# Optimization experiments

Measured on AMD Instinct MI355X. Metric: run time of the kernel, lower is better.

Reference implementation:

```python
import jax, jax.numpy as jnp
import numpy as np

B, H, W = 128, 64, 64
CH = 64            # feature channels (hardcoded self.channels=64)
GH = GW = 8        # glimpse size
HID = 128          # controller_out
NUM_GLIMPSES = 8
BN_EPS = 1e-5


def setup_inputs() -> dict:
    key = jax.random.key(0)
    ks = jax.random.split(key, 16)
    d = {}
    d['image_pairs'] = jax.random.normal(ks[0], (B, 2, H, W), dtype=jnp.float32)
    # ResidualBlock(1 -> 64)
    d['conv1_w'] = jax.random.normal(ks[1], (CH, 1, 3, 3), jnp.float32) * 0.1
    d['conv1_b'] = jnp.zeros((CH,), jnp.float32)
    d['bn1_g'] = jnp.ones((CH,), jnp.float32)
    d['bn1_b'] = jnp.zeros((CH,), jnp.float32)
    d['conv2_w'] = jax.random.normal(ks[2], (CH, CH, 3, 3), jnp.float32) * 0.02
    d['conv2_b'] = jnp.zeros((CH,), jnp.float32)
    d['bn2_g'] = jnp.ones((CH,), jnp.float32)
    d['bn2_b'] = jnp.zeros((CH,), jnp.float32)
    # LSTMCell(input=GH*GW*CH=4096, hidden=128); torch gate order i,f,g,o
    in_sz = GH * GW * CH
    d['w_ih'] = jax.random.normal(ks[3], (4 * HID, in_sz), jnp.float32) * 0.01
    d['w_hh'] = jax.random.normal(ks[4], (4 * HID, HID), jnp.float32) * 0.05
    d['b_ih'] = jnp.zeros((4 * HID,), jnp.float32)
    d['b_hh'] = jnp.zeros((4 * HID,), jnp.float32)
    # glimpser Linear(128 -> 3)
    d['glimpser_w'] = jax.random.normal(ks[5], (3, HID), jnp.float32) * 0.05
    d['glimpser_b'] = jnp.zeros((3,), jnp.float32)
    return d


def _conv3x3(x, w, b):
    # x: (B,C,H,W), w: (O,I,3,3) -> SAME padding, stride 1 (NCHW/OIHW)
    y = jax.lax.conv_general_dilated(x, w, (1, 1), 'SAME',
                                     dimension_numbers=('NCHW', 'OIHW', 'NCHW'))
    return y + b[None, :, None, None]


def _bn(x, g, b):
    # BatchNorm2d in training mode: batch statistics over (N,H,W)
    m = jnp.mean(x, axis=(0, 2, 3), keepdims=True)
    v = jnp.var(x, axis=(0, 2, 3), keepdims=True)
    return (x - m) * jax.lax.rsqrt(v + BN_EPS) * g[None, :, None, None] + b[None, :, None, None]


def _resblock(x, c1w, c1b, g1, b1, c2w, c2b, g2, b2):
    out = jax.nn.relu(_bn(_conv3x3(x, c1w, c1b), g1, b1))
    out = _bn(_conv3x3(out, c2w, c2b), g2, b2)
    # residual add broadcasts (B,1,H,W) -> (B,64,H,W), matching torch
    return jax.nn.relu(out + x)


def _filterbank(delta_caps, center_caps, image_size, glimpse_size):
    # returns (B, glimpse_size, image_size) Cauchy filterbank
    S = float(image_size)
    G = float(glimpse_size)
    centers = (S - 1.0) * (center_caps + 1.0) / 2.0          # (B,)
    deltas = S / G * (1.0 - jnp.abs(delta_caps))             # (B,)
    gammas = jnp.exp(1.0 - 2.0 * jnp.abs(delta_caps))        # (B,)
    gp = jnp.arange(glimpse_size, dtype=jnp.float32) - (G - 1.0) / 2.0
    gp = centers[:, None] + deltas[:, None] * gp[None, :]    # (B, g)
    ip = jnp.arange(image_size, dtype=jnp.float32)           # (S,)
    fx = (ip[None, None, :] - gp[:, :, None]) / gammas[:, None, None]
    fx = 1.0 / (jnp.pi * gammas[:, None, None] * (1.0 + fx * fx))  # (B, g, S)
    fx = fx / (jnp.sum(fx, axis=2, keepdims=True) + 1e-4)
    return fx


def reference(image_pairs, conv1_w, conv1_b, bn1_g, bn1_b,
              conv2_w, conv2_b, bn2_g, bn2_b,
              w_ih, w_hh, b_ih, b_hh, glimpser_w, glimpser_b):
    image_pairs = image_pairs.astype(jnp.float32)
    support = _resblock(image_pairs[:, 0:1], conv1_w, conv1_b, bn1_g, bn1_b,
                        conv2_w, conv2_b, bn2_g, bn2_b)  # (B,64,H,W)
    test = _resblock(image_pairs[:, 1:2], conv1_w, conv1_b, bn1_g, bn1_b,
                     conv2_w, conv2_b, bn2_g, bn2_b)
    bsz = image_pairs.shape[0]
    Hx = jnp.zeros((bsz, HID), jnp.float32)
    Cx = jnp.zeros((bsz, HID), jnp.float32)
    for turn in range(2 * NUM_GLIMPSES):
        imgs = support if (turn % 2) else test
        gp = jnp.tanh(Hx @ glimpser_w.T + glimpser_b)        # (B,3)
        Fh = _filterbank(gp[:, 2], gp[:, 0], imgs.shape[2], GH)  # (B,gh,H)
        Fw = _filterbank(gp[:, 2], gp[:, 1], imgs.shape[3], GW)  # (B,gw,W)
        # glimpse = Fh . image . Fw^T per channel (fused contraction)
        t = jnp.einsum('bgi,bcij->bcgj', Fh, imgs)           # (B,C,gh,W)
        gl = jnp.einsum('bcgj,bwj->bcgw', t, Fw)             # (B,C,gh,gw)
        flat = gl.reshape(bsz, -1)                           # (B, C*gh*gw)
        gates = flat @ w_ih.T + b_ih + Hx @ w_hh.T + b_hh    # (B, 4*HID)
        i, f, g, o = jnp.split(gates, 4, axis=1)
        Cx = jax.nn.sigmoid(f) * Cx + jax.nn.sigmoid(i) * jnp.tanh(g)
        Hx = jax.nn.sigmoid(o) * jnp.tanh(Cx)
    return Hx
```

## Files before the change

### kernel.cpp

```cpp
#include <hip/hip_runtime.h>
#include <math.h>

typedef unsigned short u16;
typedef unsigned int u32;
typedef short bf16x8 __attribute__((ext_vector_type(8)));
typedef float f32x4 __attribute__((ext_vector_type(4)));

#define PI_F 3.14159265358979323846f

__device__ __forceinline__ float bf2f(u16 u){ union{u32 i; float f;} v; v.i=((u32)u)<<16; return v.f; }
__device__ __forceinline__ u16 f2bf(float f){ union{u32 i; float f;} v; v.f=f; u32 r=v.i+0x7fffu+((v.i>>16)&1u); return (u16)(r>>16); }
__device__ __forceinline__ float sigf(float x){ return 1.0f/(1.0f+expf(-x)); }

__global__ __launch_bounds__(256) void wpack_kernel(const float* __restrict__ w2, u16* __restrict__ wpack)
{
  int e = blockIdx.x*256 + threadIdx.x;
  if (e >= 36864) return;
  int k  = e & 31;
  int oc = (e>>5) & 63;
  int tc = e>>11;
  int tap = tc>>1, c = tc&1;
  int ic = c*32 + k;
  wpack[e] = f2bf(w2[(size_t)(oc*64 + ic)*9 + tap]);
}

__global__ __launch_bounds__(256) void conv1_nhwc_kernel(
    const float* __restrict__ imgp, int ch,
    const float* __restrict__ w1, u16* __restrict__ out)
{
  int b = blockIdx.y, tile = blockIdx.x;
  int ty0 = (tile>>2)<<4, tx0 = (tile&3)<<4;
  int tid = threadIdx.x;
  __shared__ float patch[18*18];
  __shared__ float wsm[576];
  const float* ib = imgp + (((size_t)b*2 + ch)<<12);
  for (int e=tid; e<324; e+=256){
    int py = e/18, px = e - py*18;
    int gy = ty0+py-1, gx = tx0+px-1;
    float v = 0.f;
    if (gy>=0 && gy<64 && gx>=0 && gx<64) v = ib[(gy<<6)+gx];
    patch[e] = v;
  }
  for (int e=tid; e<576; e+=256) wsm[e] = w1[e];
  __syncthreads();
  int ty = tid>>4, tx = tid&15;
  float p[9];
  #pragma unroll
  for (int ky=0;ky<3;ky++)
    #pragma unroll
    for (int kx=0;kx<3;kx++) p[ky*3+kx] = patch[(ty+ky)*18 + tx+kx];
  u16* ob = out + ((((size_t)b<<12) + ((size_t)(ty0+ty)<<6) + (size_t)(tx0+tx))<<6);
  #pragma unroll
  for (int ocq=0; ocq<8; ocq++){
    u32 w4[4];
    #pragma unroll
    for (int pair=0; pair<4; pair++){
      float a0=0.f, a1=0.f;
      int oc0 = ocq*8 + pair*2;
      #pragma unroll
      for (int k=0;k<9;k++){ a0 += wsm[oc0*9+k]*p[k]; a1 += wsm[(oc0+1)*9+k]*p[k]; }
      w4[pair] = (u32)f2bf(a0) | ((u32)f2bf(a1)<<16);
    }
    ((uint4*)ob)[ocq] = make_uint4(w4[0],w4[1],w4[2],w4[3]);
  }
}

__device__ __forceinline__ void stats_body(const u16* __restrict__ buf, float* __restrict__ st, int blk, int tid)
{
  int c8 = (tid&7)*8;
  int pg = tid>>3;
  size_t p0 = (size_t)blk*1024 + pg;
  float s[8], s2[8];
  #pragma unroll
  for (int k=0;k<8;k++){ s[k]=0.f; s2[k]=0.f; }
  for (int it=0; it<32; it++){
    size_t p = p0 + (size_t)it*32;
    uint4 v = *(const uint4*)(buf + (p<<6) + c8);
    u32 rw[4] = {v.x,v.y,v.z,v.w};
    #pragma unroll
    for (int d=0; d<4; d++){
      float f0 = bf2f((u16)(rw[d]&0xffff));
      float f1 = bf2f((u16)(rw[d]>>16));
      s[d*2]   += f0; s2[d*2]   += f0*f0;
      s[d*2+1] += f1; s2[d*2+1] += f1*f1;
    }
  }
  #pragma unroll
  for (int off=32; off>=8; off>>=1){
    #pragma unroll
    for (int k=0;k<8;k++){ s[k] += __shfl_down(s[k], off, 64); s2[k] += __shfl_down(s2[k], off, 64); }
  }
  __shared__ float sm[128];
  if (tid<128) sm[tid]=0.f;
  __syncthreads();
  if ((tid&63) < 8){
    int cb = tid&7;
    #pragma unroll
    for (int k=0;k<8;k++){
      atomicAdd(&sm[cb*8+k], s[k]);
      atomicAdd(&sm[64+cb*8+k], s2[k]);
    }
  }
  __syncthreads();
  if (tid<128) atomicAdd(&st[tid], sm[tid]);
}

__global__ __launch_bounds__(256) void stats_nhwc_kernel(const u16* __restrict__ buf, float* __restrict__ st)
{
  stats_body(buf, st, blockIdx.x, threadIdx.x);
}

__global__ __launch_bounds__(256) void stats_pair_kernel(
    const u16* __restrict__ A, const u16* __restrict__ B,
    float* __restrict__ stA, float* __restrict__ stB)
{
  const u16* buf = (blockIdx.x < 512)? A : B;
  float* st = (blockIdx.x < 512)? stA : stB;
  stats_body(buf, st, blockIdx.x & 511, threadIdx.x);
}

__global__ __launch_bounds__(256) void conv2_mfma_kernel(
    const u16* __restrict__ in, const u16* __restrict__ wpack, u16* __restrict__ out,
    const float* __restrict__ st, const float* __restrict__ gam, const float* __restrict__ bet)
{
  int b = blockIdx.y, tile = blockIdx.x;
  int y0 = (tile>>2)*8, x0 = (tile&3)*16;
  int tid = threadIdx.x;
  int w = tid>>6, lane = tid&63;
  int m = lane&15, q = lane>>4;

  __shared__ __align__(16) u16 patch[11520];
  __shared__ float scs[64], shs[64];

  if (tid < 64){
    const float invN = 1.0f/524288.0f;
    float mean = st[tid]*invN;
    float var  = st[64+tid]*invN - mean*mean;
    float sc = gam[tid]*rsqrtf(var+1e-5f);
    scs[tid] = sc;
    shs[tid] = bet[tid] - mean*sc;
  }
  __syncthreads();

  for (int e=tid; e<1440; e+=256){
    int py = e/144; int rem = e - py*144;
    int px = rem>>3, cq = rem&7;
    int y = y0-1+py, x = x0-1+px;
    uint4 v = make_uint4(0,0,0,0);
    if (y>=0 && y<64 && x>=0 && x<64){
      uint4 raw = *(const uint4*)(in + ((((size_t)b<<12) + ((size_t)y<<6) + (size_t)x)<<6) + cq*8);
      u32 rw[4] = {raw.x, raw.y, raw.z, raw.w};
      u32 ow[4];
      #pragma unroll
      for (int d=0; d<4; d++){
        u32 o = 0;
        #pragma unroll
        for (int h=0; h<2; h++){
          int c = cq*8 + d*2 + h;
          float f = bf2f((u16)((rw[d]>>(16*h))&0xffff))*scs[c] + shs[c];
          f = fmaxf(f, 0.f);
          o |= ((u32)f2bf(f)) << (16*h);
        }
        ow[d] = o;
      }
      v = make_uint4(ow[0],ow[1],ow[2],ow[3]);
    }
    *(uint4*)(patch + ((((py<<3)+cq)*18 + px)<<3)) = v;
  }
  __syncthreads();

  f32x4 acc[2][4];
  #pragma unroll
  for (int mt=0;mt<2;mt++)
    #pragma unroll
    for (int nt=0;nt<4;nt++) acc[mt][nt] = (f32x4){0.f,0.f,0.f,0.f};

  #pragma unroll
  for (int tap=0; tap<9; tap++){
    const int dy = tap/3, dx = tap%3;
    #pragma unroll
    for (int c=0; c<2; c++){
      const int kk = tap*2 + c;
      bf16x8 bw[4];
      #pragma unroll
      for (int nt=0; nt<4; nt++)
        bw[nt] = *(const bf16x8*)(wpack + (size_t)(kk*64 + nt*16 + m)*32 + q*8);
      #pragma unroll
      for (int mt=0; mt<2; mt++){
        int py = 2*w + mt + dy;
        bf16x8 av = *(const bf16x8*)(patch + ((((py<<3) + (c<<2) + q)*18 + (m+dx))<<3));
        #pragma unroll
        for (int nt=0; nt<4; nt++)
          acc[mt][nt] = __builtin_amdgcn_mfma_f32_16x16x32_bf16(av, bw[nt], acc[mt][nt], 0,0,0);
      }
    }
  }
  __syncthreads();
  u16* etile = patch;
  #pragma unroll
  for (int mt=0; mt<2; mt++){
    int lp = (2*w+mt)*16 + q*4;
    #pragma unroll
    for (int nt=0; nt<4; nt++)
      #pragma unroll
      for (int r=0; r<4; r++)
        etile[(lp+r)*64 + nt*16 + m] = f2bf(acc[mt][nt][r]);
  }
  __syncthreads();
  int lp = tid>>1, half = tid&1;
  int y = y0 + (lp>>4), x = x0 + (lp&15);
  uint4* gdst = (uint4*)(out + ((((size_t)b<<12) + ((size_t)y<<6) + (size_t)x)<<6) + half*32);
  const uint4* lsrc = (const uint4*)(etile + lp*64 + half*32);
  gdst[0] = lsrc[0];
  gdst[1] = lsrc[1];
  gdst[2] = lsrc[2];
  gdst[3] = lsrc[3];
}

__device__ __forceinline__ void compute_params_lane(
    int b, int lane, float h0, float h1,
    const float* __restrict__ gw, const float* __restrict__ gb,
    float* __restrict__ FhT, float* __restrict__ Fw)
{
  float gpv[3];
  #pragma unroll
  for (int k=0;k<3;k++){
    float p = h0*gw[k*128+lane] + h1*gw[k*128+64+lane];
    #pragma unroll
    for (int off=32; off>0; off>>=1) p += __shfl_down(p, off, 64);
    float tot = __shfl(p, 0, 64);
    gpv[k] = tanhf(tot + gb[k]);
  }
  float ad = fabsf(gpv[2]);
  float delta = 8.0f*(1.0f-ad);
  float gamma = expf(1.0f-2.0f*ad);
  float inv_pg = 1.0f/(PI_F*gamma);
  float fi = (float)lane;
  float ctr = 31.5f*(gpv[0]+1.0f);
  float fh[8];
  #pragma unroll
  for (int g=0; g<8; g++){
    float mu = ctr + delta*((float)g - 3.5f);
    float u = (fi - mu)/gamma;
    float f = inv_pg/(1.0f+u*u);
    float s = f;
    #pragma unroll
    for (int off=32; off>0; off>>=1) s += __shfl_down(s, off, 64);
    s = __shfl(s, 0, 64);
    fh[g] = f/(s + 1e-4f);
  }
  float4* o = (float4*)(FhT + (((size_t)b<<6) + lane)*8);
  o[0] = make_float4(fh[0],fh[1],fh[2],fh[3]);
  o[1] = make_float4(fh[4],fh[5],fh[6],fh[7]);
  ctr = 31.5f*(gpv[1]+1.0f);
  #pragma unroll
  for (int wv=0; wv<8; wv++){
    float mu = ctr + delta*((float)wv - 3.5f);
    float u = (fi - mu)/gamma;
    float f = inv_pg/(1.0f+u*u);
    float s = f;
    #pragma unroll
    for (int off=32; off>0; off>>=1) s += __shfl_down(s, off, 64);
    s = __shfl(s, 0, 64);
    Fw[(((size_t)b<<3)+wv)*64 + lane] = f/(s + 1e-4f);
  }
}

__device__ __forceinline__ void compute_params_lds(
    int lane, int jc, const float* __restrict__ hnew,
    const float* __restrict__ gw, const float* __restrict__ gb,
    float* __restrict__ fh_lds, float* __restrict__ fw_lds)
{
  float h0 = hnew[lane], h1 = hnew[64+lane];
  float gpv[3];
  #pragma unroll
  for (int k=0;k<3;k++){
    float p = h0*gw[k*128+lane] + h1*gw[k*128+64+lane];
    #pragma unroll
    for (int off=32; off>0; off>>=1) p += __shfl_down(p, off, 64);
    float tot = __shfl(p, 0, 64);
    gpv[k] = tanhf(tot + gb[k]);
  }
  float ad = fabsf(gpv[2]);
  float delta = 8.0f*(1.0f-ad);
  float gamma = expf(1.0f-2.0f*ad);
  float inv_pg = 1.0f/(PI_F*gamma);
  float fi = (float)lane;
  float ctr = 31.5f*(gpv[0]+1.0f);
  #pragma unroll
  for (int g=0; g<8; g++){
    float mu = ctr + delta*((float)g - 3.5f);
    float u = (fi - mu)/gamma;
    float f = inv_pg/(1.0f+u*u);
    float s = f;
    #pragma unroll
    for (int off=32; off>0; off>>=1) s += __shfl_down(s, off, 64);
    s = __shfl(s, 0, 64);
    fh_lds[lane*8+g] = f/(s + 1e-4f);
  }
  ctr = 31.5f*(gpv[1]+1.0f);
  #pragma unroll
  for (int wv=0; wv<8; wv++){
    float mu = ctr + delta*((float)wv - 3.5f);
    float u = (fi - mu)/gamma;
    float f = inv_pg/(1.0f+u*u);
    float s = f;
    #pragma unroll
    for (int off=32; off>0; off>>=1) s += __shfl_down(s, off, 64);
    s = __shfl(s, 0, 64);
    int jl = lane - jc*16;
    if (jl >= 0 && jl < 16) fw_lds[jl*8+wv] = f/(s + 1e-4f);
  }
}

__global__ __launch_bounds__(256) void glimpse_lstm_kernel(
    const u16* __restrict__ img, const float* __restrict__ part,
    const float* __restrict__ whhT,
    const float* __restrict__ bih, const float* __restrict__ bhh,
    const float* __restrict__ gw, const float* __restrict__ gb,
    const float* __restrict__ Hx_in, const float* __restrict__ Cx_in,
    float* __restrict__ Hx_out, float* __restrict__ Cx_out,
    float* __restrict__ part_gl,
    const float* __restrict__ st2, const float* __restrict__ gam2,
    const float* __restrict__ bet2, const float* __restrict__ imgp,
    int ch, int t)
{
  int jc = blockIdx.x, b = blockIdx.y;
  int tid = threadIdx.x;
  __shared__ float hs[128];
  __shared__ float hnew[128];
  __shared__ float gsm[512];
  __shared__ float scs[64], shs[64];
  __shared__ __align__(16) float fh_lds[512];
  __shared__ __align__(16) float fw_lds[128];
  __shared__ __align__(16) float t_lds[8*16*64];

  if (tid < 64){
    const float invN = 1.0f/524288.0f;
    float mean = st2[tid]*invN;
    float var  = st2[64+tid]*invN - mean*mean;
    float sc = gam2[tid]*rsqrtf(var+1e-5f);
    scs[tid] = sc;
    shs[tid] = bet2[tid] - mean*sc;
  }

  if (t > 0){
    if (tid < 128) hs[tid] = Hx_in[b*128+tid];
    __syncthreads();
    #pragma unroll
    for (int gq=0; gq<2; gq++){
      int n = gq*256 + tid;
      float acc = bih[n] + bhh[n];
      const float* pp = part + (size_t)b*16384 + n;
      #pragma unroll 8
      for (int ks=0; ks<32; ks++) acc += pp[ks*512];
      const float* wp = whhT + n;
      #pragma unroll 8
      for (int k=0;k<128;k++) acc += hs[k]*wp[(size_t)k*512];
      gsm[n] = acc;
    }
    __syncthreads();
    if (tid < 128){
      float cx = Cx_in[b*128+tid];
      float cn = sigf(gsm[128+tid])*cx + sigf(gsm[tid])*tanhf(gsm[256+tid]);
      float hn = sigf(gsm[384+tid])*tanhf(cn);
      hnew[tid] = hn;
      if (jc == 0){ Cx_out[b*128+tid] = cn; Hx_out[b*128+tid] = hn; }
    }
  } else {
    if (tid < 128) hnew[tid] = 0.f;
  }
  __syncthreads();

  if (tid < 64) compute_params_lds(tid, jc, hnew, gw, gb, fh_lds, fw_lds);
  __syncthreads();

  int ih = tid>>7, j = (tid>>3)&15, cg = tid&7;
  float scq[8], shq[8];
  #pragma unroll
  for (int k=0;k<8;k++){ scq[k] = scs[cg*8+k]; shq[k] = shs[cg*8+k]; }
  f32x4 accA[8], accB[8];
  #pragma unroll
  for (int g=0;g<8;g++){ accA[g]=(f32x4){0.f,0.f,0.f,0.f}; accB[g]=(f32x4){0.f,0.f,0.f,0.f}; }
  const u16* ib = img + ((((size_t)b<<12) + ((size_t)(ih*32)<<6) + (size_t)(jc*16+j))<<6) + cg*8;
  const float* rp = imgp + (((size_t)(b*2+ch))<<12) + ((size_t)(ih*32)<<6) + (jc*16+j);
  #pragma unroll 8
  for (int ii=0; ii<32; ii++){
    uint4 vv = *(const uint4*)(ib + ((size_t)ii<<12));
    float res = rp[ii<<6];
    float x0=fmaxf(bf2f((u16)(vv.x&0xffff))*scq[0]+shq[0]+res, 0.f);
    float x1=fmaxf(bf2f((u16)(vv.x>>16))   *scq[1]+shq[1]+res, 0.f);
    float x2=fmaxf(bf2f((u16)(vv.y&0xffff))*scq[2]+shq[2]+res, 0.f);
    float x3=fmaxf(bf2f((u16)(vv.y>>16))   *scq[3]+shq[3]+res, 0.f);
    float x4=fmaxf(bf2f((u16)(vv.z&0xffff))*scq[4]+shq[4]+res, 0.f);
    float x5=fmaxf(bf2f((u16)(vv.z>>16))   *scq[5]+shq[5]+res, 0.f);
    float x6=fmaxf(bf2f((u16)(vv.w&0xffff))*scq[6]+shq[6]+res, 0.f);
    float x7=fmaxf(bf2f((u16)(vv.w>>16))   *scq[7]+shq[7]+res, 0.f);
    int i = ih*32+ii;
    f32x4 fa = *(const f32x4*)&fh_lds[i*8];
    f32x4 fb = *(const f32x4*)&fh_lds[i*8+4];
    #pragma unroll
    for (int g=0;g<4;g++){
      accA[g][0]+=fa[g]*x0; accA[g][1]+=fa[g]*x1; accA[g][2]+=fa[g]*x2; accA[g][3]+=fa[g]*x3;
      accB[g][0]+=fa[g]*x4; accB[g][1]+=fa[g]*x5; accB[g][2]+=fa[g]*x6; accB[g][3]+=fa[g]*x7;
      accA[g+4][0]+=fb[g]*x0; accA[g+4][1]+=fb[g]*x1; accA[g+4][2]+=fb[g]*x2; accA[g+4][3]+=fb[g]*x3;
      accB[g+4][0]+=fb[g]*x4; accB[g+4][1]+=fb[g]*x5; accB[g+4][2]+=fb[g]*x6; accB[g+4][3]+=fb[g]*x7;
    }
  }
  if (ih==0){
    #pragma unroll
    for (int g=0;g<8;g++){
      *(f32x4*)&t_lds[(g*16+j)*64 + cg*8]     = accA[g];
      *(f32x4*)&t_lds[(g*16+j)*64 + cg*8 + 4] = accB[g];
    }
  }
  __syncthreads();
  if (ih==1){
    #pragma unroll
    for (int g=0;g<8;g++){
      f32x4* p0 = (f32x4*)&t_lds[(g*16+j)*64 + cg*8];
      p0[0] = p0[0] + accA[g];
      p0[1] = p0[1] + accB[g];
    }
  }
  __syncthreads();

  int c = tid&63, s = tid>>6;
  float acc2[2][8];
  #pragma unroll
  for (int gi=0;gi<2;gi++)
    #pragma unroll
    for (int wv=0;wv<8;wv++) acc2[gi][wv]=0.f;
  #pragma unroll
  for (int jl=0; jl<16; jl++){
    float tv0 = t_lds[((((s*2  )<<4)+jl)<<6) + c];
    float tv1 = t_lds[((((s*2+1)<<4)+jl)<<6) + c];
    f32x4 w0 = *(const f32x4*)&fw_lds[jl*8];
    f32x4 w1 = *(const f32x4*)&fw_lds[jl*8+4];
    acc2[0][0]+=tv0*w0[0]; acc2[0][1]+=tv0*w0[1]; acc2[0][2]+=tv0*w0[2]; acc2[0][3]+=tv0*w0[3];
    acc2[0][4]+=tv0*w1[0]; acc2[0][5]+=tv0*w1[1]; acc2[0][6]+=tv0*w1[2]; acc2[0][7]+=tv0*w1[3];
    acc2[1][0]+=tv1*w0[0]; acc2[1][1]+=tv1*w0[1]; acc2[1][2]+=tv1*w0[2]; acc2[1][3]+=tv1*w0[3];
    acc2[1][4]+=tv1*w1[0]; acc2[1][5]+=tv1*w1[1]; acc2[1][6]+=tv1*w1[2]; acc2[1][7]+=tv1*w1[3];
  }
  float* dst = part_gl + (((size_t)(b*4+jc))<<12) + c*64 + (s*2)*8;
  *(f32x4*)(dst+0)  = (f32x4){acc2[0][0],acc2[0][1],acc2[0][2],acc2[0][3]};
  *(f32x4*)(dst+4)  = (f32x4){acc2[0][4],acc2[0][5],acc2[0][6],acc2[0][7]};
  *(f32x4*)(dst+8)  = (f32x4){acc2[1][0],acc2[1][1],acc2[1][2],acc2[1][3]};
  *(f32x4*)(dst+12) = (f32x4){acc2[1][4],acc2[1][5],acc2[1][6],acc2[1][7]};
}

__global__ __launch_bounds__(256) void gemm_ih_kernel(
    const float* __restrict__ part_gl, const float* __restrict__ Bw, float* __restrict__ part)
{
  int n0 = blockIdx.x*64;
  int kb = blockIdx.y;
  int k0 = kb*128;
  __shared__ __align__(16) float Asm[16*132];
  __shared__ __align__(16) float Bsm[16*68];
  int tid = threadIdx.x;
  int tm = tid & 15, tn = tid >> 4;
  float acc[8][4];
  #pragma unroll
  for (int i=0;i<8;i++)
    #pragma unroll
    for (int jj=0;jj<4;jj++) acc[i][jj]=0.f;
  for (int kt=0; kt<128; kt+=16){
    for (int e=tid; e<512; e+=256){
      int mrow = e>>2, kq = e&3;
      const float* pg = part_gl + ((size_t)mrow<<14) + (k0+kt+kq*4);
      float4 a0 = *(const float4*)pg;
      float4 a1 = *(const float4*)(pg+4096);
      float4 a2 = *(const float4*)(pg+8192);
      float4 a3 = *(const float4*)(pg+12288);
      float4 a = make_float4(a0.x+a1.x+a2.x+a3.x, a0.y+a1.y+a2.y+a3.y,
                             a0.z+a1.z+a2.z+a3.z, a0.w+a1.w+a2.w+a3.w);
      Asm[(kq*4+0)*132+mrow] = a.x;
      Asm[(kq*4+1)*132+mrow] = a.y;
      Asm[(kq*4+2)*132+mrow] = a.z;
      Asm[(kq*4+3)*132+mrow] = a.w;
    }
    {
      int e = tid;
      int n = e>>2, kq = e&3;
      float4 bv = *(const float4*)(Bw + (size_t)(n0+n)*4096 + k0+kt+kq*4);
      Bsm[(kq*4+0)*68+n] = bv.x;
      Bsm[(kq*4+1)*68+n] = bv.y;
      Bsm[(kq*4+2)*68+n] = bv.z;
      Bsm[(kq*4+3)*68+n] = bv.w;
    }
    __syncthreads();
    #pragma unroll
    for (int kk=0;kk<16;kk++){
      float4 bv = *(const float4*)&Bsm[kk*68 + tn*4];
      float4 a0 = *(const float4*)&Asm[kk*132 + tm*8];
      float4 a1 = *(const float4*)&Asm[kk*132 + tm*8 + 4];
      float av[8] = {a0.x,a0.y,a0.z,a0.w,a1.x,a1.y,a1.z,a1.w};
      #pragma unroll
      for (int mm=0;mm<8;mm++){
        acc[mm][0] += av[mm]*bv.x;
        acc[mm][1] += av[mm]*bv.y;
        acc[mm][2] += av[mm]*bv.z;
        acc[mm][3] += av[mm]*bv.w;
      }
    }
    __syncthreads();
  }
  #pragma unroll
  for (int mm=0;mm<8;mm++){
    int mrow = tm*8+mm;
    *(float4*)&part[(size_t)mrow*16384 + kb*512 + n0 + tn*4] =
        make_float4(acc[mm][0],acc[mm][1],acc[mm][2],acc[mm][3]);
  }
}

__global__ __launch_bounds__(256) void lstm_update_kernel(
    float* __restrict__ Hx, float* __restrict__ Cx,
    const float* __restrict__ part, const float* __restrict__ whhT,
    const float* __restrict__ b_ih, const float* __restrict__ b_hh,
    const float* __restrict__ gw, const float* __restrict__ gb,
    float* __restrict__ FhT, float* __restrict__ Fw)
{
  int b = blockIdx.x;
  int tid = threadIdx.x;
  int hid = tid & 127, half = tid >> 7;
  __shared__ float hs[128];
  __shared__ float hs2[128];
  __shared__ float gp[1024];
  if (tid < 128) hs[tid] = Hx[b*128+tid];
  __syncthreads();
  #pragma unroll
  for (int qd=0; qd<4; qd++){
    int n = qd*128 + hid;
    float acc = half ? 0.f : (b_ih[n] + b_hh[n]);
    const float* pp = part + (size_t)b*16384 + (size_t)(half*16)*512 + n;
    #pragma unroll
    for (int ks=0; ks<16; ks++) acc += pp[ks*512];
    const float* wp = whhT + n + (size_t)(half*64)*512;
    const float* hp = hs + half*64;
    #pragma unroll 8
    for (int k=0;k<64;k++) acc += hp[k]*wp[(size_t)k*512];
    gp[(half*4+qd)*128 + hid] = acc;
  }
  __syncthreads();
  if (tid < 128){
    float g0 = gp[  0+tid] + gp[512+  0+tid];
    float g1 = gp[128+tid] + gp[512+128+tid];
    float g2 = gp[256+tid] + gp[512+256+tid];
    float g3 = gp[384+tid] + gp[512+384+tid];
    float cx = Cx[b*128+tid];
    float cn = sigf(g1)*cx + sigf(g0)*tanhf(g2);
    float hn = sigf(g3)*tanhf(cn);
    Cx[b*128+tid] = cn;
    Hx[b*128+tid] = hn;
    hs2[tid] = hn;
  }
  __syncthreads();
  if (tid < 64)
    compute_params_lane(b, tid, hs2[tid], hs2[64+tid], gw, gb, FhT, Fw);
}

__global__ __launch_bounds__(256) void transpose_whh_kernel(
    const float* __restrict__ whh, float* __restrict__ whhT)
{
  int idx = blockIdx.x*256 + threadIdx.x;
  int k = idx>>9, n = idx&511;
  whhT[idx] = whh[n*128 + k];
}

extern "C" void kernel_launch(void* const* d_in, const int* in_sizes, int n_in,
                              void* d_out, int out_size, void* d_ws, size_t ws_size,
                              hipStream_t stream)
{
  const float* imgp = (const float*)d_in[0];
  const float* w1  = (const float*)d_in[1];
  const float* g1  = (const float*)d_in[3];
  const float* be1 = (const float*)d_in[4];
  const float* w2  = (const float*)d_in[5];
  const float* g2  = (const float*)d_in[7];
  const float* be2 = (const float*)d_in[8];
  const float* wih = (const float*)d_in[9];
  const float* whh = (const float*)d_in[10];
  const float* bih = (const float*)d_in[11];
  const float* bhh = (const float*)d_in[12];
  const float* gw  = (const float*)d_in[13];
  const float* gb  = (const float*)d_in[14];

  char* ws = (char*)d_ws;
  u16* imgT    = (u16*)(ws + 0);
  u16* imgS    = (u16*)(ws + 67108864);
  u16* tmp     = (u16*)(ws + 134217728);
  float* Hbuf1   = (float*)(ws + 134217728);
  float* cbuf1   = (float*)(ws + 134283264);
  float* part_gl = (float*)(ws + 134742016);
  float* part    = (float*)(ws + 143130624);
  float* whhT    = (float*)(ws + 151519232);
  u16*   wpack   = (u16*)  (ws + 201326592);
  float* Hbuf0   = (float*)(ws + 201400320);
  float* cbuf0   = (float*)(ws + 201465856);
  float* stats   = (float*)(ws + 201531392);
  if (ws_size < 201533440ull) return;

  hipMemsetAsync(Hbuf0, 0, 65536+65536+2048, stream);
  wpack_kernel<<<144,256,0,stream>>>(w2, wpack);

  for (int s=0; s<2; s++){
    int ch = (s==0)?1:0;
    u16* dst = (s==0)? imgT : imgS;
    conv1_nhwc_kernel<<<dim3(16,128),256,0,stream>>>(imgp, ch, w1, tmp);
    stats_nhwc_kernel<<<512,256,0,stream>>>(tmp, stats + 128*(2*s));
    conv2_mfma_kernel<<<dim3(32,128),256,0,stream>>>(tmp, wpack, dst,
        stats + 128*(2*s), g1, be1);
  }
  stats_pair_kernel<<<1024,256,0,stream>>>(imgT, imgS, stats + 128, stats + 384);

  transpose_whh_kernel<<<256,256,0,stream>>>(whh, whhT);

  for (int t=0; t<16; t++){
    int sup = t&1;
    const u16* im = sup? imgS : imgT;
    const float* st2 = sup? (stats+384) : (stats+128);
    int ch = sup? 0 : 1;
    const float* Hin = sup? Hbuf0 : Hbuf1;
    const float* Cin = sup? cbuf0 : cbuf1;
    float* Hout = sup? Hbuf1 : Hbuf0;
    float* Cout = sup? cbuf1 : cbuf0;
    glimpse_lstm_kernel<<<dim3(4,128),256,0,stream>>>(
        im, part, whhT, bih, bhh, gw, gb, Hin, Cin, Hout, Cout, part_gl,
        st2, g2, be2, imgp, ch, t);
    gemm_ih_kernel<<<dim3(8,32),256,0,stream>>>(part_gl, wih, part);
  }
  lstm_update_kernel<<<128,256,0,stream>>>(Hbuf1, cbuf1, part, whhT, bih, bhh, gw, gb,
                                           part_gl, part_gl + 65536 );

  hipMemcpyAsync(d_out, Hbuf1, (size_t)16384*4, hipMemcpyDeviceToDevice, stream);
}
```

Before: 1.511 ms.

## Shrink per-block work in conv2, glimpse and input GEMM kernels to add parallelism

The conv2 MFMA kernel now covers 4-row tiles instead of 8, with each wave computing one row, and launches twice as many blocks. The glimpse/LSTM kernel moves to 512 threads, so each thread handles 16 rows instead of 32 and the extra partial sums are reduced through LDS. The input-projection GEMM halves its N tile to 32 and doubles its grid. The aim is higher occupancy and more blocks on a latency-bound pipeline, at the cost of more halo loads, extra LDS reduction passes with barriers, and less reuse per block.

```diff
diff --git a/kernel.cpp b/kernel.cpp
--- a/kernel.cpp
+++ b/kernel.cpp
@@ -119,17 +119,17 @@
   stats_body(buf, st, blockIdx.x & 511, threadIdx.x);
 }
 
-__global__ __launch_bounds__(256) void conv2_mfma_kernel(
+__global__ __launch_bounds__(256,6) void conv2_mfma_kernel(
     const u16* __restrict__ in, const u16* __restrict__ wpack, u16* __restrict__ out,
     const float* __restrict__ st, const float* __restrict__ gam, const float* __restrict__ bet)
 {
   int b = blockIdx.y, tile = blockIdx.x;
-  int y0 = (tile>>2)*8, x0 = (tile&3)*16;
+  int y0 = (tile>>2)*4, x0 = (tile&3)*16;
   int tid = threadIdx.x;
   int w = tid>>6, lane = tid&63;
   int m = lane&15, q = lane>>4;
 
-  __shared__ __align__(16) u16 patch[11520];
+  __shared__ __align__(16) u16 patch[6912];
   __shared__ float scs[64], shs[64];
 
   if (tid < 64){
@@ -142,7 +142,7 @@
   }
   __syncthreads();
 
-  for (int e=tid; e<1440; e+=256){
+  for (int e=tid; e<864; e+=256){
     int py = e/144; int rem = e - py*144;
     int px = rem>>3, cq = rem&7;
     int y = y0-1+py, x = x0-1+px;
@@ -169,11 +169,9 @@
   }
   __syncthreads();
 
-  f32x4 acc[2][4];
-  #pragma unroll
-  for (int mt=0;mt<2;mt++)
-    #pragma unroll
-    for (int nt=0;nt<4;nt++) acc[mt][nt] = (f32x4){0.f,0.f,0.f,0.f};
+  f32x4 acc[4];
+  #pragma unroll
+  for (int nt=0;nt<4;nt++) acc[nt] = (f32x4){0.f,0.f,0.f,0.f};
 
   #pragma unroll
   for (int tap=0; tap<9; tap++){
@@ -185,36 +183,34 @@
       #pragma unroll
       for (int nt=0; nt<4; nt++)
         bw[nt] = *(const bf16x8*)(wpack + (size_t)(kk*64 + nt*16 + m)*32 + q*8);
+      int py = w + dy;
+      bf16x8 av = *(const bf16x8*)(patch + ((((py<<3) + (c<<2) + q)*18 + (m+dx))<<3));
       #pragma unroll
-      for (int mt=0; mt<2; mt++){
-        int py = 2*w + mt + dy;
-        bf16x8 av = *(const bf16x8*)(patch + ((((py<<3) + (c<<2) + q)*18 + (m+dx))<<3));
-        #pragma unroll
-        for (int nt=0; nt<4; nt++)
-          acc[mt][nt] = __builtin_amdgcn_mfma_f32_16x16x32_bf16(av, bw[nt], acc[mt][nt], 0,0,0);
-      }
+      for (int nt=0; nt<4; nt++)
+        acc[nt] = __builtin_amdgcn_mfma_f32_16x16x32_bf16(av, bw[nt], acc[nt], 0,0,0);
     }
   }
   __syncthreads();
   u16* etile = patch;
-  #pragma unroll
-  for (int mt=0; mt<2; mt++){
-    int lp = (2*w+mt)*16 + q*4;
+  {
+    int lp = w*16 + q*4;
     #pragma unroll
     for (int nt=0; nt<4; nt++)
       #pragma unroll
       for (int r=0; r<4; r++)
-        etile[(lp+r)*64 + nt*16 + m] = f2bf(acc[mt][nt][r]);
-  }
-  __syncthreads();
-  int lp = tid>>1, half = tid&1;
-  int y = y0 + (lp>>4), x = x0 + (lp&15);
-  uint4* gdst = (uint4*)(out + ((((size_t)b<<12) + ((size_t)y<<6) + (size_t)x)<<6) + half*32);
-  const uint4* lsrc = (const uint4*)(etile + lp*64 + half*32);
-  gdst[0] = lsrc[0];
-  gdst[1] = lsrc[1];
-  gdst[2] = lsrc[2];
-  gdst[3] = lsrc[3];
+        etile[(lp+r)*64 + nt*16 + m] = f2bf(acc[nt][r]);
+  }
+  __syncthreads();
+  if (tid < 128){
+    int lp = tid>>1, half = tid&1;
+    int y = y0 + (lp>>4), x = x0 + (lp&15);
+    uint4* gdst = (uint4*)(out + ((((size_t)b<<12) + ((size_t)y<<6) + (size_t)x)<<6) + half*32);
+    const uint4* lsrc = (const uint4*)(etile + lp*64 + half*32);
+    gdst[0] = lsrc[0];
+    gdst[1] = lsrc[1];
+    gdst[2] = lsrc[2];
+    gdst[3] = lsrc[3];
+  }
 }
 
 __device__ __forceinline__ void compute_params_lane(
@@ -313,7 +309,7 @@
   }
 }
 
-__global__ __launch_bounds__(256) void glimpse_lstm_kernel(
+__global__ __launch_bounds__(512,4) void glimpse_lstm_kernel(
     const u16* __restrict__ img, const float* __restrict__ part,
     const float* __restrict__ whhT,
     const float* __restrict__ bih, const float* __restrict__ bhh,
@@ -347,9 +343,8 @@
   if (t > 0){
     if (tid < 128) hs[tid] = Hx_in[b*128+tid];
     __syncthreads();
-    #pragma unroll
-    for (int gq=0; gq<2; gq++){
-      int n = gq*256 + tid;
+    {
+      int n = tid;
       float acc = bih[n] + bhh[n];
       const float* pp = part + (size_t)b*16384 + n;
       #pragma unroll 8
@@ -382,10 +377,10 @@
   f32x4 accA[8], accB[8];
   #pragma unroll
   for (int g=0;g<8;g++){ accA[g]=(f32x4){0.f,0.f,0.f,0.f}; accB[g]=(f32x4){0.f,0.f,0.f,0.f}; }
-  const u16* ib = img + ((((size_t)b<<12) + ((size_t)(ih*32)<<6) + (size_t)(jc*16+j))<<6) + cg*8;
-  const float* rp = imgp + (((size_t)(b*2+ch))<<12) + ((size_t)(ih*32)<<6) + (jc*16+j);
+  const u16* ib = img + ((((size_t)b<<12) + ((size_t)(ih*16)<<6) + (size_t)(jc*16+j))<<6) + cg*8;
+  const float* rp = imgp + (((size_t)(b*2+ch))<<12) + ((size_t)(ih*16)<<6) + (jc*16+j);
   #pragma unroll 8
-  for (int ii=0; ii<32; ii++){
+  for (int ii=0; ii<16; ii++){
     uint4 vv = *(const uint4*)(ib + ((size_t)ii<<12));
     float res = rp[ii<<6];
     float x0=fmaxf(bf2f((u16)(vv.x&0xffff))*scq[0]+shq[0]+res, 0.f);
@@ -396,7 +391,7 @@
     float x5=fmaxf(bf2f((u16)(vv.z>>16))   *scq[5]+shq[5]+res, 0.f);
     float x6=fmaxf(bf2f((u16)(vv.w&0xffff))*scq[6]+shq[6]+res, 0.f);
     float x7=fmaxf(bf2f((u16)(vv.w>>16))   *scq[7]+shq[7]+res, 0.f);
-    int i = ih*32+ii;
+    int i = ih*16+ii;
     f32x4 fa = *(const f32x4*)&fh_lds[i*8];
     f32x4 fb = *(const f32x4*)&fh_lds[i*8+4];
     #pragma unroll
@@ -424,46 +419,57 @@
     }
   }
   __syncthreads();
-
-  int c = tid&63, s = tid>>6;
-  float acc2[2][8];
-  #pragma unroll
-  for (int gi=0;gi<2;gi++)
-    #pragma unroll
-    for (int wv=0;wv<8;wv++) acc2[gi][wv]=0.f;
-  #pragma unroll
-  for (int jl=0; jl<16; jl++){
-    float tv0 = t_lds[((((s*2  )<<4)+jl)<<6) + c];
-    float tv1 = t_lds[((((s*2+1)<<4)+jl)<<6) + c];
-    f32x4 w0 = *(const f32x4*)&fw_lds[jl*8];
-    f32x4 w1 = *(const f32x4*)&fw_lds[jl*8+4];
-    acc2[0][0]+=tv0*w0[0]; acc2[0][1]+=tv0*w0[1]; acc2[0][2]+=tv0*w0[2]; acc2[0][3]+=tv0*w0[3];
-    acc2[0][4]+=tv0*w1[0]; acc2[0][5]+=tv0*w1[1]; acc2[0][6]+=tv0*w1[2]; acc2[0][7]+=tv0*w1[3];
-    acc2[1][0]+=tv1*w0[0]; acc2[1][1]+=tv1*w0[1]; acc2[1][2]+=tv1*w0[2]; acc2[1][3]+=tv1*w0[3];
-    acc2[1][4]+=tv1*w1[0]; acc2[1][5]+=tv1*w1[1]; acc2[1][6]+=tv1*w1[2]; acc2[1][7]+=tv1*w1[3];
-  }
-  float* dst = part_gl + (((size_t)(b*4+jc))<<12) + c*64 + (s*2)*8;
-  *(f32x4*)(dst+0)  = (f32x4){acc2[0][0],acc2[0][1],acc2[0][2],acc2[0][3]};
-  *(f32x4*)(dst+4)  = (f32x4){acc2[0][4],acc2[0][5],acc2[0][6],acc2[0][7]};
-  *(f32x4*)(dst+8)  = (f32x4){acc2[1][0],acc2[1][1],acc2[1][2],acc2[1][3]};
-  *(f32x4*)(dst+12) = (f32x4){acc2[1][4],acc2[1][5],acc2[1][6],acc2[1][7]};
+  if (ih==2){
+    #pragma unroll
+    for (int g=0;g<8;g++){
+      f32x4* p0 = (f32x4*)&t_lds[(g*16+j)*64 + cg*8];
+      p0[0] = p0[0] + accA[g];
+      p0[1] = p0[1] + accB[g];
+    }
+  }
+  __syncthreads();
+  if (ih==3){
+    #pragma unroll
+    for (int g=0;g<8;g++){
+      f32x4* p0 = (f32x4*)&t_lds[(g*16+j)*64 + cg*8];
+      p0[0] = p0[0] + accA[g];
+      p0[1] = p0[1] + accB[g];
+    }
+  }
+  __syncthreads();
+
+  {
+    int c = tid&63, s = tid>>6;
+    float acc2[8];
+    #pragma unroll
+    for (int wv=0;wv<8;wv++) acc2[wv]=0.f;
+    #pragma unroll
+    for (int jl=0; jl<16; jl++){
+      float tv = t_lds[(((s<<4)+jl)<<6) + c];
+      f32x4 w0 = *(const f32x4*)&fw_lds[jl*8];
+      f32x4 w1 = *(const f32x4*)&fw_lds[jl*8+4];
+      acc2[0]+=tv*w0[0]; acc2[1]+=tv*w0[1]; acc2[2]+=tv*w0[2]; acc2[3]+=tv*w0[3];
+      acc2[4]+=tv*w1[0]; acc2[5]+=tv*w1[1]; acc2[6]+=tv*w1[2]; acc2[7]+=tv*w1[3];
+    }
+    float* dst = part_gl + (((size_t)(b*4+jc))<<12) + c*64 + s*8;
+    *(f32x4*)(dst+0) = (f32x4){acc2[0],acc2[1],acc2[2],acc2[3]};
+    *(f32x4*)(dst+4) = (f32x4){acc2[4],acc2[5],acc2[6],acc2[7]};
+  }
 }
 
 __global__ __launch_bounds__(256) void gemm_ih_kernel(
     const float* __restrict__ part_gl, const float* __restrict__ Bw, float* __restrict__ part)
 {
-  int n0 = blockIdx.x*64;
+  int n0 = blockIdx.x*32;
   int kb = blockIdx.y;
   int k0 = kb*128;
   __shared__ __align__(16) float Asm[16*132];
-  __shared__ __align__(16) float Bsm[16*68];
+  __shared__ __align__(16) float Bsm[16*36];
   int tid = threadIdx.x;
   int tm = tid & 15, tn = tid >> 4;
-  float acc[8][4];
-  #pragma unroll
-  for (int i=0;i<8;i++)
-    #pragma unroll
-    for (int jj=0;jj<4;jj++) acc[i][jj]=0.f;
+  float acc[8][2];
+  #pragma unroll
+  for (int i=0;i<8;i++){ acc[i][0]=0.f; acc[i][1]=0.f; }
   for (int kt=0; kt<128; kt+=16){
     for (int e=tid; e<512; e+=256){
       int mrow = e>>2, kq = e&3;
@@ -479,28 +485,26 @@
       Asm[(kq*4+2)*132+mrow] = a.z;
       Asm[(kq*4+3)*132+mrow] = a.w;
     }
-    {
-      int e = tid;
-      int n = e>>2, kq = e&3;
+    if (tid < 128){
+      int n = tid>>2, kq = tid&3;
       float4 bv = *(const float4*)(Bw + (size_t)(n0+n)*4096 + k0+kt+kq*4);
-      Bsm[(kq*4+0)*68+n] = bv.x;
-      Bsm[(kq*4+1)*68+n] = bv.y;
-      Bsm[(kq*4+2)*68+n] = bv.z;
-      Bsm[(kq*4+3)*68+n] = bv.w;
+      Bsm[(kq*4+0)*36+n] = bv.x;
+      Bsm[(kq*4+1)*36+n] = bv.y;
+      Bsm[(kq*4+2)*36+n] = bv.z;
+      Bsm[(kq*4+3)*36+n] = bv.w;
     }
     __syncthreads();
     #pragma unroll
     for (int kk=0;kk<16;kk++){
-      float4 bv = *(const float4*)&Bsm[kk*68 + tn*4];
+      float b0 = Bsm[kk*36 + tn*2];
+      float b1 = Bsm[kk*36 + tn*2 + 1];
       float4 a0 = *(const float4*)&Asm[kk*132 + tm*8];
       float4 a1 = *(const float4*)&Asm[kk*132 + tm*8 + 4];
       float av[8] = {a0.x,a0.y,a0.z,a0.w,a1.x,a1.y,a1.z,a1.w};
       #pragma unroll
       for (int mm=0;mm<8;mm++){
-        acc[mm][0] += av[mm]*bv.x;
-        acc[mm][1] += av[mm]*bv.y;
-        acc[mm][2] += av[mm]*bv.z;
-        acc[mm][3] += av[mm]*bv.w;
+        acc[mm][0] += av[mm]*b0;
+        acc[mm][1] += av[mm]*b1;
       }
     }
     __syncthreads();
@@ -508,8 +512,8 @@
   #pragma unroll
   for (int mm=0;mm<8;mm++){
     int mrow = tm*8+mm;
-    *(float4*)&part[(size_t)mrow*16384 + kb*512 + n0 + tn*4] =
-        make_float4(acc[mm][0],acc[mm][1],acc[mm][2],acc[mm][3]);
+    *(float2*)&part[(size_t)mrow*16384 + kb*512 + n0 + tn*2] =
+        make_float2(acc[mm][0],acc[mm][1]);
   }
 }
 
@@ -608,7 +612,7 @@
     u16* dst = (s==0)? imgT : imgS;
     conv1_nhwc_kernel<<<dim3(16,128),256,0,stream>>>(imgp, ch, w1, tmp);
     stats_nhwc_kernel<<<512,256,0,stream>>>(tmp, stats + 128*(2*s));
-    conv2_mfma_kernel<<<dim3(32,128),256,0,stream>>>(tmp, wpack, dst,
+    conv2_mfma_kernel<<<dim3(64,128),256,0,stream>>>(tmp, wpack, dst,
         stats + 128*(2*s), g1, be1);
   }
   stats_pair_kernel<<<1024,256,0,stream>>>(imgT, imgS, stats + 128, stats + 384);
@@ -624,10 +628,10 @@
     const float* Cin = sup? cbuf0 : cbuf1;
     float* Hout = sup? Hbuf1 : Hbuf0;
     float* Cout = sup? cbuf1 : cbuf0;
-    glimpse_lstm_kernel<<<dim3(4,128),256,0,stream>>>(
+    glimpse_lstm_kernel<<<dim3(4,128),512,0,stream>>>(
         im, part, whhT, bih, bhh, gw, gb, Hin, Cin, Hout, Cout, part_gl,
         st2, g2, be2, imgp, ch, t);
-    gemm_ih_kernel<<<dim3(8,32),256,0,stream>>>(part_gl, wih, part);
+    gemm_ih_kernel<<<dim3(16,32),256,0,stream>>>(part_gl, wih, part);
   }
   lstm_update_kernel<<<128,256,0,stream>>>(Hbuf1, cbuf1, part, whhT, bih, bhh, gw, gb,
                                            part_gl, part_gl + 65536 );
```

Measured after the change: 1.520 ms. Within noise of the previous version (+0.6%).
